# Kernel tuning notes

Hardware: AMD Instinct MI355X
Metric: run time of the kernel (lower is better)

Reference implementation:

```python
import jax, jax.numpy as jnp
import numpy as np

B, C, H, W = 256, 256, 14, 14
CH = C // 2  # 128
N = H * W    # 196
EPS = 1e-5


def setup_inputs() -> dict:
    key = jax.random.key(0)
    ks = jax.random.split(key, 8)
    return {
        "x": jax.random.normal(ks[0], (B, C, H, W), jnp.float32),
        "y": jax.random.normal(ks[1], (B, C, H, W), jnp.float32),
        "Wq": jax.random.normal(ks[2], (CH, C), jnp.float32) * 0.05,
        "Wk": jax.random.normal(ks[3], (CH, C), jnp.float32) * 0.05,
        "Wv": jax.random.normal(ks[4], (CH, C), jnp.float32) * 0.05,
        "Wz": jax.random.normal(ks[5], (C, CH), jnp.float32) * 0.05,
        "bn_weight": jnp.ones((C,), jnp.float32),
        "bn_bias": jnp.zeros((C,), jnp.float32),
        "bn_mean": jax.random.normal(ks[6], (C,), jnp.float32) * 0.1,
        "bn_var": jax.random.uniform(ks[7], (C,), jnp.float32, 0.5, 1.5),
    }


def reference(x, y, Wq, Wk, Wv, Wz, bn_weight, bn_bias, bn_mean, bn_var):
    b = x.shape[0]
    xf = x.reshape(b, C, N)  # [B, C, N]
    yf = y.reshape(b, C, N)
    # 1x1 convs == channel matmuls
    Q = jnp.einsum('oc,bcn->bon', Wq, xf)  # [B, CH, N]
    K = jnp.einsum('oc,bcn->bon', Wk, yf)
    V = jnp.einsum('oc,bcn->bon', Wv, yf)
    # M = Q^T K  -> [B, N, N]
    M = jnp.einsum('bcq,bck->bqk', Q, K)
    # Softmax2d over a singleton channel dim (faithful to original: yields ones)
    M = jax.nn.softmax(M[:, None, :, :], axis=1)[:, 0]
    Z = jnp.einsum('bcn,bnm->bcm', V, M)  # [B, CH, N]
    Z = jnp.einsum('oc,bcn->bon', Wz, Z)  # [B, C, N]
    Z = Z.reshape(b, C, H, W)
    # BatchNorm2d (inference form with running stats)
    inv = jax.lax.rsqrt(bn_var + EPS)
    Z = (Z - bn_mean[:, None, None]) * (inv * bn_weight)[:, None, None] + bn_bias[:, None, None]
    return x + Z
```

## Files before the change

### kernel.cpp

```cpp
#include <hip/hip_runtime.h>
#include <hip/hip_bf16.h>

#define B_  256
#define C_  256
#define CH_ 128
#define N_  196
#define NF4 49
#define EPS 1e-5f

__global__ __launch_bounds__(256) void k_ysum(const float* __restrict__ y,
                                              float* __restrict__ ysum) {
    int wave = blockIdx.x * 4 + (threadIdx.x >> 6);
    int lane = threadIdx.x & 63;
    const float4* row = (const float4*)(y + (size_t)wave * N_);
    float s = 0.f;
    if (lane < NF4) {
        float4 v = row[lane];
        s = (v.x + v.y) + (v.z + v.w);
    }
    #pragma unroll
    for (int off = 32; off > 0; off >>= 1)
        s += __shfl_down(s, off, 64);
    if (lane == 0) ysum[wave] = s;
}

__global__ __launch_bounds__(256) void k_wzvt(const float* __restrict__ Wz,
                                              const float* __restrict__ Wv,
                                              float* __restrict__ WzvT) {
    __shared__ float sWv[CH_];
    int c = blockIdx.x;
    int o = threadIdx.x;
    if (o < CH_) sWv[o] = Wv[o * C_ + c];
    __syncthreads();
    const float4* wzrow = (const float4*)(Wz + o * CH_);
    float acc = 0.f;
    #pragma unroll
    for (int k4 = 0; k4 < CH_ / 4; k4++) {
        float4 w = wzrow[k4];
        acc += w.x * sWv[4 * k4 + 0];
        acc += w.y * sWv[4 * k4 + 1];
        acc += w.z * sWv[4 * k4 + 2];
        acc += w.w * sWv[4 * k4 + 3];
    }
    WzvT[c * C_ + o] = acc;
}

__global__ __launch_bounds__(256) void k_z2(const float* __restrict__ ysum,
                                            const float* __restrict__ WzvT,
                                            const float* __restrict__ bnw,
                                            const float* __restrict__ bnb,
                                            const float* __restrict__ bnm,
                                            const float* __restrict__ bnv,
                                            float* __restrict__ Zs) {
    __shared__ float sY[C_];
    int b = blockIdx.x;
    int o = threadIdx.x;
    sY[o] = ysum[b * C_ + o];
    __syncthreads();
    float acc = 0.f;
    #pragma unroll 8
    for (int c = 0; c < C_; c++)
        acc += sY[c] * WzvT[c * C_ + o];
    float alpha = bnw[o] * rsqrtf(bnv[o] + EPS);
    Zs[b * C_ + o] = (acc - bnm[o]) * alpha + bnb[o];
}

__global__ __launch_bounds__(256) void k_out(const float* __restrict__ x,
                                             const float* __restrict__ Zs,
                                             float* __restrict__ out) {
    int idx = blockIdx.x * blockDim.x + threadIdx.x;
    int row = idx / NF4;
    float z = Zs[row];
    float4 v = ((const float4*)x)[idx];
    v.x += z; v.y += z; v.z += z; v.w += z;
    ((float4*)out)[idx] = v;
}

extern "C" void kernel_launch(void* const* d_in, const int* in_sizes, int n_in,
                              void* d_out, int out_size, void* d_ws, size_t ws_size,
                              hipStream_t stream) {
    const float* x   = (const float*)d_in[0];
    const float* y   = (const float*)d_in[1];
    const float* Wv  = (const float*)d_in[4];
    const float* Wz  = (const float*)d_in[5];
    const float* bnw = (const float*)d_in[6];
    const float* bnb = (const float*)d_in[7];
    const float* bnm = (const float*)d_in[8];
    const float* bnv = (const float*)d_in[9];
    float* out = (float*)d_out;

    float* ysum = (float*)d_ws;
    float* WzvT = ysum + B_ * C_;
    float* Zs   = WzvT + C_ * C_;

    k_ysum<<<(B_ * C_) / 4, 256, 0, stream>>>(y, ysum);
    k_wzvt<<<C_, 256, 0, stream>>>(Wz, Wv, WzvT);
    k_z2<<<B_, 256, 0, stream>>>(ysum, WzvT, bnw, bnb, bnm, bnv, Zs);
    k_out<<<(B_ * C_ * NF4) / 256, 256, 0, stream>>>(x, Zs, out);
}
```

Measured before the change: 171.6 us.

## Fuse four kernels into two: merged precompute and fused Z-GEMV with residual add

Combines the y row-sum and the Wz·Wv weight-product kernels into one launch using block-index dispatch. It also fuses the per-batch Z computation (GEMV plus BatchNorm) into the final residual-add kernel. Each block handles a quarter of a batch's channels, splitting the K reduction across four waves and staging results in shared memory. This removes two launches and the Zs round trip through global memory. In exchange the GEMV runs with only 1024 blocks and each block does some redundant loading of ysum.

```diff
diff --git a/kernel.cpp b/kernel.cpp
--- a/kernel.cpp
+++ b/kernel.cpp
@@ -1,79 +1,107 @@
 #include <hip/hip_runtime.h>
 #include <hip/hip_bf16.h>
 
-#define B_  256
-#define C_  256
-#define CH_ 128
-#define N_  196
-#define NF4 49
+#define B_   256
+#define C_   256
+#define CH_  128
+#define N_   196
+#define NF4  49
+#define ROWS (B_ * C_)
+#define YSUM_BLKS (ROWS / 4)
+#define QF4  (64 * NF4)
 #define EPS 1e-5f
 
-__global__ __launch_bounds__(256) void k_ysum(const float* __restrict__ y,
-                                              float* __restrict__ ysum) {
-    int wave = blockIdx.x * 4 + (threadIdx.x >> 6);
-    int lane = threadIdx.x & 63;
-    const float4* row = (const float4*)(y + (size_t)wave * N_);
-    float s = 0.f;
-    if (lane < NF4) {
-        float4 v = row[lane];
-        s = (v.x + v.y) + (v.z + v.w);
+__global__ __launch_bounds__(256) void k_pre(const float* __restrict__ y,
+                                             const float* __restrict__ Wz,
+                                             const float* __restrict__ Wv,
+                                             float* __restrict__ ysum,
+                                             float* __restrict__ WzvT) {
+    int bid = blockIdx.x;
+    if (bid < YSUM_BLKS) {
+        int wave = bid * 4 + (threadIdx.x >> 6);
+        int lane = threadIdx.x & 63;
+        const float4* row = (const float4*)(y + (size_t)wave * N_);
+        float s = 0.f;
+        if (lane < NF4) {
+            float4 v = row[lane];
+            s = (v.x + v.y) + (v.z + v.w);
+        }
+        #pragma unroll
+        for (int off = 32; off > 0; off >>= 1)
+            s += __shfl_down(s, off, 64);
+        if (lane == 0) ysum[wave] = s;
+    } else {
+        __shared__ float sWv[CH_];
+        int c = bid - YSUM_BLKS;
+        int o = threadIdx.x;
+        if (o < CH_) sWv[o] = Wv[o * C_ + c];
+        __syncthreads();
+        const float4* wzrow = (const float4*)(Wz + o * CH_);
+        float acc = 0.f;
+        #pragma unroll
+        for (int k4 = 0; k4 < CH_ / 4; k4++) {
+            float4 w = wzrow[k4];
+            acc += w.x * sWv[4 * k4 + 0];
+            acc += w.y * sWv[4 * k4 + 1];
+            acc += w.z * sWv[4 * k4 + 2];
+            acc += w.w * sWv[4 * k4 + 3];
+        }
+        WzvT[c * C_ + o] = acc;
     }
-    #pragma unroll
-    for (int off = 32; off > 0; off >>= 1)
-        s += __shfl_down(s, off, 64);
-    if (lane == 0) ysum[wave] = s;
 }
 
-__global__ __launch_bounds__(256) void k_wzvt(const float* __restrict__ Wz,
-                                              const float* __restrict__ Wv,
-                                              float* __restrict__ WzvT) {
-    __shared__ float sWv[CH_];
-    int c = blockIdx.x;
-    int o = threadIdx.x;
-    if (o < CH_) sWv[o] = Wv[o * C_ + c];
+__global__ __launch_bounds__(256) void k_post(const float* __restrict__ x,
+                                              const float* __restrict__ ysum,
+                                              const float* __restrict__ WzvT,
+                                              const float* __restrict__ bnw,
+                                              const float* __restrict__ bnb,
+                                              const float* __restrict__ bnm,
+                                              const float* __restrict__ bnv,
+                                              float* __restrict__ out) {
+    __shared__ float sY[C_];
+    __shared__ float sP[4][64];
+    __shared__ float sZ[64];
+
+    int b = blockIdx.x >> 2;
+    int q = blockIdx.x & 3;
+    int t = threadIdx.x;
+
+    sY[t] = ysum[b * C_ + t];
     __syncthreads();
-    const float4* wzrow = (const float4*)(Wz + o * CH_);
-    float acc = 0.f;
+
+    int c_local = t & 63;
+    int slice   = t >> 6;
+    int c       = q * 64 + c_local;
+    {
+        float acc = 0.f;
+        const float* wcol = WzvT + c;
+        int k0 = slice * 64;
+        #pragma unroll 8
+        for (int k = k0; k < k0 + 64; k++)
+            acc += sY[k] * wcol[k * C_];
+        sP[slice][c_local] = acc;
+    }
+    __syncthreads();
+    if (t < 64) {
+        float z = (sP[0][t] + sP[1][t]) + (sP[2][t] + sP[3][t]);
+        int cc = q * 64 + t;
+        float alpha = bnw[cc] * rsqrtf(bnv[cc] + EPS);
+        sZ[t] = (z - bnm[cc]) * alpha + bnb[cc];
+    }
+    __syncthreads();
+
+    const float4* xb = (const float4*)x  + (size_t)blockIdx.x * QF4;
+    float4*       ob = (float4*)out      + (size_t)blockIdx.x * QF4;
     #pragma unroll
-    for (int k4 = 0; k4 < CH_ / 4; k4++) {
-        float4 w = wzrow[k4];
-        acc += w.x * sWv[4 * k4 + 0];
-        acc += w.y * sWv[4 * k4 + 1];
-        acc += w.z * sWv[4 * k4 + 2];
-        acc += w.w * sWv[4 * k4 + 3];
+    for (int it = 0; it < 13; it++) {
+        int i = it * 256 + t;
+        if (i < QF4) {
+            float z = sZ[i / NF4];
+            float4 v = xb[i];
+            v.x += z; v.y += z; v.z += z; v.w += z;
+            ob[i] = v;
+        }
     }
-    WzvT[c * C_ + o] = acc;
-}
-
-__global__ __launch_bounds__(256) void k_z2(const float* __restrict__ ysum,
-                                            const float* __restrict__ WzvT,
-                                            const float* __restrict__ bnw,
-                                            const float* __restrict__ bnb,
-                                            const float* __restrict__ bnm,
-                                            const float* __restrict__ bnv,
-                                            float* __restrict__ Zs) {
-    __shared__ float sY[C_];
-    int b = blockIdx.x;
-    int o = threadIdx.x;
-    sY[o] = ysum[b * C_ + o];
-    __syncthreads();
-    float acc = 0.f;
-    #pragma unroll 8
-    for (int c = 0; c < C_; c++)
-        acc += sY[c] * WzvT[c * C_ + o];
-    float alpha = bnw[o] * rsqrtf(bnv[o] + EPS);
-    Zs[b * C_ + o] = (acc - bnm[o]) * alpha + bnb[o];
-}
-
-__global__ __launch_bounds__(256) void k_out(const float* __restrict__ x,
-                                             const float* __restrict__ Zs,
-                                             float* __restrict__ out) {
-    int idx = blockIdx.x * blockDim.x + threadIdx.x;
-    int row = idx / NF4;
-    float z = Zs[row];
-    float4 v = ((const float4*)x)[idx];
-    v.x += z; v.y += z; v.z += z; v.w += z;
-    ((float4*)out)[idx] = v;
 }
 
 extern "C" void kernel_launch(void* const* d_in, const int* in_sizes, int n_in,
@@ -91,10 +119,7 @@
 
     float* ysum = (float*)d_ws;
     float* WzvT = ysum + B_ * C_;
-    float* Zs   = WzvT + C_ * C_;
 
-    k_ysum<<<(B_ * C_) / 4, 256, 0, stream>>>(y, ysum);
-    k_wzvt<<<C_, 256, 0, stream>>>(Wz, Wv, WzvT);
-    k_z2<<<B_, 256, 0, stream>>>(ysum, WzvT, bnw, bnb, bnm, bnv, Zs);
-    k_out<<<(B_ * C_ * NF4) / 256, 256, 0, stream>>>(x, Zs, out);
+    k_pre<<<YSUM_BLKS + C_, 256, 0, stream>>>(y, Wz, Wv, ysum, WzvT);
+    k_post<<<B_ * 4, 256, 0, stream>>>(x, ysum, WzvT, bnw, bnb, bnm, bnv, out);
 }
```

Result: slower. 176.8 us (+3.0%).
